# Optimization experiments

Hardware: AMD Instinct MI355X
Metric: run time of the kernel (lower is better)

Reference implementation:

```python
import jax, jax.numpy as jnp
import numpy as np

U = 512   # units
D = 512   # decoder input feature dim
V = 46    # output vocab


def _lstm_cell(x_t, h, c, W, R, b):
    # Keras LSTMCell: gate order i, f, g(cell), o; sigmoid recurrent act, tanh act.
    z = x_t @ W + h @ R + b                      # [B, 4U]
    i, f, g, o = jnp.split(z, 4, axis=-1)
    i = jax.nn.sigmoid(i)
    f = jax.nn.sigmoid(f)
    g = jnp.tanh(g)
    o = jax.nn.sigmoid(o)
    c_new = f * c + i * g
    h_new = o * jnp.tanh(c_new)
    return h_new, c_new


def _lstm_seq(seq, W, R, b):
    # seq: [T, B, D]; zero initial state (Keras default). Returns (all h [T,B,U], last h [B,U]).
    B = seq.shape[1]
    u = R.shape[0]
    h0 = jnp.zeros((B, u), seq.dtype)
    c0 = jnp.zeros((B, u), seq.dtype)
    def step(carry, x_t):
        h, c = carry
        h, c = _lstm_cell(x_t, h, c, W, R, b)
        return (h, c), h
    (hT, _), hs = jax.lax.scan(step, (h0, c0), seq)
    return hs, hT


def setup_inputs() -> dict:
    key = jax.random.key(0)
    ks = jax.random.split(key, 10)
    def p(k, shape, scale=0.05):
        return jax.random.normal(k, shape, dtype=jnp.float32) * scale
    x = jax.random.normal(ks[0], (32, 512, U), dtype=jnp.float32)   # encoder outputs [B, S, U]
    y = jax.random.normal(ks[1], (32, 128, D), dtype=jnp.float32)   # decoder inputs  [B, T, D]
    return {
        "x": x, "y": y,
        "W_a": p(ks[2], (D, 4 * U)), "R_a": p(ks[3], (U, 4 * U)), "b_a": jnp.zeros((4 * U,), jnp.float32),
        "W1": p(ks[4], (U, 4 * U)), "R1": p(ks[5], (U, 4 * U)), "b1": jnp.zeros((4 * U,), jnp.float32),
        "W2": p(ks[6], (U, 4 * U)), "R2": p(ks[7], (U, 4 * U)), "b2": jnp.zeros((4 * U,), jnp.float32),
        "Wd": p(ks[8], (U, V)), "bd": jnp.zeros((V,), jnp.float32),
    }


def reference(x, y, W_a, R_a, b_a, W1, R1, b1, W2, R2, b2, Wd, bd):
    B = y.shape[0]
    yT = jnp.swapaxes(y, 0, 1)                          # [T, B, D]
    h0 = jnp.zeros((B, U), x.dtype)
    c0 = jnp.zeros((B, U), x.dtype)

    # AttentionLSTM: per-step LSTMCell + dot-product attention (Keras Attention,
    # unscaled, keys==values==x) + residual add of the context into both states.
    def step(carry, y_t):
        h, c = carry
        h, c = _lstm_cell(y_t, h, c, W_a, R_a, b_a)     # s = h  [B, U]
        scores = jnp.einsum('bu,bsu->bs', h, x)         # [B, S]
        ctx = jnp.einsum('bs,bsu->bu', jax.nn.softmax(scores, axis=-1), x)  # [B, U]
        return (h + ctx, c + ctx), ctx

    _, ctxs = jax.lax.scan(step, (h0, c0), yT)          # [T, B, U]

    # Stacked LSTMs: first returns full sequence, second returns last hidden state.
    hs1, _ = _lstm_seq(ctxs, W1, R1, b1)                # [T, B, U]
    _, hT = _lstm_seq(hs1, W2, R2, b2)                  # [B, U]

    logits = hT @ Wd + bd                               # [B, V]
    return jax.nn.softmax(logits, axis=-1)
```

## Files before the change

### kernel.cpp

```cpp
#include <hip/hip_runtime.h>
#include <math.h>


#define U_   512
#define S_   512
#define T_   128
#define B_   32
#define G4   2048
#define V_   46
#define NWG  256
#define FSTR 32

#define AT_LD(p)     __hip_atomic_load((p), __ATOMIC_RELAXED, __HIP_MEMORY_SCOPE_AGENT)
#define AT_ST(p, v)  __hip_atomic_store((p), (v), __ATOMIC_RELAXED, __HIP_MEMORY_SCOPE_AGENT)

__device__ __forceinline__ void group_bar(unsigned* gflags, unsigned seq) {
  __syncthreads();
  const int tid = threadIdx.x;
  if (tid < 32) {
    if (tid == 0)
      AT_ST(&gflags[(blockIdx.x & 31) * FSTR], seq);
    while (!__all(AT_LD(&gflags[tid * FSTR]) >= seq))
      __builtin_amdgcn_s_sleep(1);
  }
  __syncthreads();
}

__global__ __launch_bounds__(256) void gemm_k512(
    const float* __restrict__ A, const float* __restrict__ W,
    const float* __restrict__ b, float* __restrict__ Z) {
  const int tid = threadIdx.x;
  const int j = blockIdx.x * 1024 + tid * 4;
  const int i0 = blockIdx.y * 8;
  float4 bj = *(const float4*)(b + j);
  float4 acc[8];
#pragma unroll
  for (int r = 0; r < 8; ++r) acc[r] = bj;
  const float* Arow = A + (size_t)i0 * U_;
  for (int k = 0; k < U_; ++k) {
    float4 w = *(const float4*)(W + (size_t)k * G4 + j);
#pragma unroll
    for (int r = 0; r < 8; ++r) {
      float a = Arow[(size_t)r * U_ + k];
      acc[r].x = fmaf(a, w.x, acc[r].x);
      acc[r].y = fmaf(a, w.y, acc[r].y);
      acc[r].z = fmaf(a, w.z, acc[r].z);
      acc[r].w = fmaf(a, w.w, acc[r].w);
    }
  }
#pragma unroll
  for (int r = 0; r < 8; ++r)
    *(float4*)(Z + (size_t)(i0 + r) * G4 + j) = acc[r];
}

__global__ __launch_bounds__(256) void transpose_R(
    const float* __restrict__ R, float* __restrict__ RT) {
  __shared__ float tile[64][65];
  const int c0 = blockIdx.x * 64, k0 = blockIdx.y * 64;
  const int tc = threadIdx.x & 63, tr = threadIdx.x >> 6;
  for (int r = tr; r < 64; r += 4)
    tile[r][tc] = R[(size_t)(k0 + r) * G4 + c0 + tc];
  __syncthreads();
  for (int r = tr; r < 64; r += 4)
    RT[(size_t)(c0 + r) * 512 + k0 + tc] = tile[tc][r];
}

__global__ __launch_bounds__(512) void attn_coop(
    const float* __restrict__ x, const float* __restrict__ ZY,
    const float* __restrict__ RT, float* __restrict__ ctxs,
    float* hbuf, float* hnbuf, float* smax, float* ssumg,
    float* ctxpart, unsigned* flags) {
  extern __shared__ float dyn[];
  float* x_s  = dyn;
  float* h_st = dyn + 512 * 65;
  __shared__ float zp[4][64][2];
  __shared__ float p_s[64];
  __shared__ float ctx_s[64];

  const int tid = threadIdx.x;
  const int bid = blockIdx.x;
  const int g    = bid >> 5;
  const int wgid = bid & 31;
  const int u0   = wgid * 16;
  const int kh  = tid & 1;
  const int b_l = (tid >> 1) & 3;
  const int col = tid >> 3;
  const int zcol = (col >> 4) * 512 + u0 + (col & 15);
  const int b_att = 4 * g + (wgid >> 3);
  const int sc = wgid & 7;
  unsigned* gflags = flags + g * 32 * FSTR;

  for (int idx = tid; idx < 64 * 512; idx += 512) {
    int sl = idx >> 9, u = idx & 511;
    x_s[u * 65 + sl] = x[((size_t)b_att * S_ + sc * 64 + sl) * U_ + u];
  }
  float c = 0.f, hn_reg = 0.f;
  unsigned seq = 0;
  __syncthreads();

  for (int t = 0; t < T_; ++t) {
    {
      float4 v = make_float4(0.f, 0.f, 0.f, 0.f);
      if (t) {
        const float4* hb4 =
            (const float4*)(hbuf + (size_t)t * 16384 + 4 * g * 512);
        v = hb4[tid];
      }
      *(float4*)(h_st + (tid >> 7) * 516 + (tid & 127) * 4) = v;
    }
    __syncthreads();
    {
      const float4* H4 = (const float4*)(h_st + b_l * 516 + kh * 256);
      const float4* R4 = (const float4*)(RT + (size_t)zcol * 512 + kh * 256);
      float acc = 0.f;
#pragma unroll 8
      for (int i = 0; i < 64; ++i) {
        float4 hv = H4[i];
        float4 rv = R4[i];
        acc = fmaf(hv.x, rv.x, acc); acc = fmaf(hv.y, rv.y, acc);
        acc = fmaf(hv.z, rv.z, acc); acc = fmaf(hv.w, rv.w, acc);
      }
      zp[b_l][col][kh] = acc;
    }
    __syncthreads();
    if (tid < 64) {
      const int bb = tid >> 4, uu = tid & 15;
      const int b = 4 * g + bb, u = u0 + uu;
      const float* zy = ZY + ((size_t)b * T_ + t) * G4 + u;
      float zi = zy[0]    + zp[bb][uu][0]      + zp[bb][uu][1];
      float zf = zy[512]  + zp[bb][16 + uu][0] + zp[bb][16 + uu][1];
      float zg = zy[1024] + zp[bb][32 + uu][0] + zp[bb][32 + uu][1];
      float zo = zy[1536] + zp[bb][48 + uu][0] + zp[bb][48 + uu][1];
      float ig = 1.f / (1.f + expf(-zi));
      float fg = 1.f / (1.f + expf(-zf));
      float gg = tanhf(zg);
      float og = 1.f / (1.f + expf(-zo));
      c = fg * c + ig * gg;
      hn_reg = og * tanhf(c);
      AT_ST(&hnbuf[(size_t)t * 16384 + b * 512 + u], hn_reg);
    }
    group_bar(gflags, ++seq);

    {
      const int wv = tid >> 6, ln = tid & 63;
      const float* hnb = hnbuf + (size_t)t * 16384 + b_att * 512;
      float hreg[8];
#pragma unroll
      for (int k = 0; k < 8; ++k) hreg[k] = hnb[ln + 64 * k];
      for (int si = 0; si < 8; ++si) {
        const int sl = wv * 8 + si;
        float a = 0.f;
#pragma unroll
        for (int k = 0; k < 8; ++k)
          a = fmaf(hreg[k], x_s[(ln + 64 * k) * 65 + sl], a);
#pragma unroll
        for (int off = 32; off; off >>= 1) a += __shfl_down(a, off);
        if (ln == 0) p_s[sl] = a;
      }
    }
    __syncthreads();
    if (tid < 64) {
      float v = p_s[tid];
      float m = v;
#pragma unroll
      for (int off = 32; off; off >>= 1) m = fmaxf(m, __shfl_down(m, off));
      m = __shfl(m, 0);
      float ex = expf(v - m);
      p_s[tid] = ex;
      float sm = ex;
#pragma unroll
      for (int off = 32; off; off >>= 1) sm += __shfl_down(sm, off);
      if (tid == 0) {
        AT_ST(&smax[b_att * 8 + sc], m);
        AT_ST(&ssumg[b_att * 8 + sc], sm);
      }
    }
    __syncthreads();
    {
      float a = 0.f;
      const float* xr = x_s + tid * 65;
#pragma unroll 8
      for (int s = 0; s < 64; ++s) a = fmaf(p_s[s], xr[s], a);
      AT_ST(&ctxpart[((size_t)b_att * 8 + sc) * 512 + tid], a);
    }
    group_bar(gflags, ++seq);

    {
      const int j = tid & 7;
      const int pair = tid >> 3;
      const int bb = pair >> 4, uu = pair & 15;
      const int b = 4 * g + bb, u = u0 + uu;
      float lm = AT_LD(&smax[b * 8 + j]);
      float ss = AT_LD(&ssumg[b * 8 + j]);
      float cp = AT_LD(&ctxpart[((size_t)b * 8 + j) * 512 + u]);
      float gm = lm;
#pragma unroll
      for (int off = 1; off < 8; off <<= 1)
        gm = fmaxf(gm, __shfl_xor(gm, off));
      float w = expf(lm - gm);
      float st = ss * w, cs = cp * w;
#pragma unroll
      for (int off = 1; off < 8; off <<= 1) {
        st += __shfl_xor(st, off);
        cs += __shfl_xor(cs, off);
      }
      if (j == 0) ctx_s[pair] = cs / st;
    }
    __syncthreads();
    if (tid < 64) {
      const int bb = tid >> 4, uu = tid & 15;
      const int b = 4 * g + bb, u = u0 + uu;
      float ctxv = ctx_s[tid];
      c += ctxv;
      float hcar = hn_reg + ctxv;
      AT_ST(&hbuf[(size_t)(t + 1) * 16384 + b * 512 + u], hcar);
      ctxs[((size_t)b * T_ + t) * U_ + u] = ctxv;
    }
    group_bar(gflags, ++seq);
  }
}

__global__ __launch_bounds__(512) void lstm_coop(
    const float* __restrict__ Zin, const float* __restrict__ R,
    float* __restrict__ seq_out, float* hbuf, unsigned* flags,
    const float* __restrict__ Wd, const float* __restrict__ bd,
    float* __restrict__ out) {
  extern __shared__ float dyn[];
  float* R_s  = dyn;
  float* h_st = dyn + 64 * 516;
  __shared__ float zp[4][64][2];
  const int tid = threadIdx.x;
  const int bid = blockIdx.x;
  const int g    = bid >> 5;
  const int wgid = bid & 31;
  const int u0   = wgid * 16;
  const int kh  = tid & 1;
  const int b_l = (tid >> 1) & 3;
  const int col = tid >> 3;
  unsigned* gflags = flags + g * 32 * FSTR;

  for (int idx = tid; idx < 64 * 512; idx += 512) {
    int cc = idx & 63, kk = idx >> 6;
    R_s[cc * 516 + kk] = R[(size_t)kk * G4 + (cc >> 4) * 512 + u0 + (cc & 15)];
  }
  float c = 0.f;
  unsigned seq = 0;
  __syncthreads();

  for (int t = 0; t < T_; ++t) {
    {
      float4 v = make_float4(0.f, 0.f, 0.f, 0.f);
      if (t) {
        const float4* hb4 =
            (const float4*)(hbuf + (size_t)t * 16384 + 4 * g * 512);
        v = hb4[tid];
      }
      *(float4*)(h_st + (tid >> 7) * 516 + (tid & 127) * 4) = v;
    }
    __syncthreads();
    {
      const float4* H4 = (const float4*)(h_st + b_l * 516 + kh * 256);
      const float4* R4 = (const float4*)(R_s + col * 516 + kh * 256);
      float acc = 0.f;
#pragma unroll 8
      for (int i = 0; i < 64; ++i) {
        float4 hv = H4[i];
        float4 rv = R4[i];
        acc = fmaf(hv.x, rv.x, acc); acc = fmaf(hv.y, rv.y, acc);
        acc = fmaf(hv.z, rv.z, acc); acc = fmaf(hv.w, rv.w, acc);
      }
      zp[b_l][col][kh] = acc;
    }
    __syncthreads();
    if (tid < 64) {
      const int bb = tid >> 4, uu = tid & 15;
      const int b = 4 * g + bb, u = u0 + uu;
      const float* zy = Zin + ((size_t)b * T_ + t) * G4 + u;
      float zi = zy[0]    + zp[bb][uu][0]      + zp[bb][uu][1];
      float zf = zy[512]  + zp[bb][16 + uu][0] + zp[bb][16 + uu][1];
      float zg = zy[1024] + zp[bb][32 + uu][0] + zp[bb][32 + uu][1];
      float zo = zy[1536] + zp[bb][48 + uu][0] + zp[bb][48 + uu][1];
      float ig = 1.f / (1.f + expf(-zi));
      float fg = 1.f / (1.f + expf(-zf));
      float gg = tanhf(zg);
      float og = 1.f / (1.f + expf(-zo));
      c = fg * c + ig * gg;
      float hv2 = og * tanhf(c);
      AT_ST(&hbuf[(size_t)(t + 1) * 16384 + b * 512 + u], hv2);
      if (seq_out) seq_out[((size_t)b * T_ + t) * U_ + u] = hv2;
    }
    group_bar(gflags, ++seq);
  }

  if (Wd && wgid == 0 && tid < 256) {
    const int b = 4 * g + (tid >> 6);
    const int v = tid & 63;
    const float* hT = hbuf + (size_t)T_ * 16384 + (size_t)b * 512;
    float acc = (v < V_) ? bd[v] : -INFINITY;
    if (v < V_) {
      for (int k = 0; k < U_; ++k)
        acc = fmaf(hT[k], Wd[(size_t)k * V_ + v], acc);
    }
    float m = acc;
#pragma unroll
    for (int off = 32; off; off >>= 1) m = fmaxf(m, __shfl_down(m, off));
    m = __shfl(m, 0);
    float e = (v < V_) ? expf(acc - m) : 0.f;
    float s = e;
#pragma unroll
    for (int off = 32; off; off >>= 1) s += __shfl_down(s, off);
    s = __shfl(s, 0);
    if (v < V_) out[(size_t)b * V_ + v] = e / s;
  }
}

extern "C" void kernel_launch(void* const* d_in, const int* in_sizes, int n_in,
                              void* d_out, int out_size, void* d_ws, size_t ws_size,
                              hipStream_t stream) {
  const float* x   = (const float*)d_in[0];
  const float* y   = (const float*)d_in[1];
  const float* W_a = (const float*)d_in[2];
  const float* R_a = (const float*)d_in[3];
  const float* b_a = (const float*)d_in[4];
  const float* W1  = (const float*)d_in[5];
  const float* R1  = (const float*)d_in[6];
  const float* b1  = (const float*)d_in[7];
  const float* W2  = (const float*)d_in[8];
  const float* R2  = (const float*)d_in[9];
  const float* b2  = (const float*)d_in[10];
  const float* Wd  = (const float*)d_in[11];
  const float* bd  = (const float*)d_in[12];
  float* out = (float*)d_out;

  float* ZBUF  = (float*)d_ws;
  float* SEQ   = ZBUF + (size_t)8388608;
  float* RT    = SEQ + (size_t)2097152;
  float* HROT  = RT + (size_t)1048576;
  float* HNROT = HROT + (size_t)2113536;
  float* SMAX  = HNROT + (size_t)2097152;
  float* SSUM  = SMAX + 256;
  float* CTXP  = SSUM + 256;
  float* HT    = CTXP + 131072;
  unsigned* BAR = (unsigned*)(HT + 16384);

  const int REGION = 8 * 32 * FSTR;
  unsigned* FLG_A = BAR;
  unsigned* FLG_1 = BAR + REGION;
  unsigned* FLG_2 = BAR + 2 * REGION;

  const int attn_lds = (512 * 65 + 4 * 516) * 4;
  const int lstm_lds = (64 * 516 + 4 * 516) * 4;
  hipFuncSetAttribute((const void*)attn_coop,
                      hipFuncAttributeMaxDynamicSharedMemorySize, attn_lds);
  hipFuncSetAttribute((const void*)lstm_coop,
                      hipFuncAttributeMaxDynamicSharedMemorySize, lstm_lds);

  dim3 ggrid(2, 512);
  hipMemsetAsync(BAR, 0, 3 * REGION * 4, stream);

  gemm_k512<<<ggrid, 256, 0, stream>>>(y, W_a, b_a, ZBUF);
  transpose_R<<<dim3(32, 8), 256, 0, stream>>>(R_a, RT);
  attn_coop<<<NWG, 512, attn_lds, stream>>>(x, ZBUF, RT, SEQ, HROT, HNROT,
                                            SMAX, SSUM, CTXP, FLG_A);
  gemm_k512<<<ggrid, 256, 0, stream>>>(SEQ, W1, b1, ZBUF);
  lstm_coop<<<NWG, 512, lstm_lds, stream>>>(ZBUF, R1, SEQ, HROT, FLG_1,
                                            nullptr, nullptr, nullptr);
  gemm_k512<<<ggrid, 256, 0, stream>>>(SEQ, W2, b2, ZBUF);
  lstm_coop<<<NWG, 512, lstm_lds, stream>>>(ZBUF, R2, nullptr, HROT, FLG_2,
                                            Wd, bd, out);
}
```

Baseline: 4.037 ms.

## Fuse attention and both stacked LSTMs into one wavefront-pipelined persistent kernel

```diff
diff --git a/kernel.cpp b/kernel.cpp
--- a/kernel.cpp
+++ b/kernel.cpp
@@ -8,23 +8,10 @@
 #define B_   32
 #define G4   2048
 #define V_   46
-#define NWG  256
 #define FSTR 32
 
 #define AT_LD(p)     __hip_atomic_load((p), __ATOMIC_RELAXED, __HIP_MEMORY_SCOPE_AGENT)
 #define AT_ST(p, v)  __hip_atomic_store((p), (v), __ATOMIC_RELAXED, __HIP_MEMORY_SCOPE_AGENT)
-
-__device__ __forceinline__ void group_bar(unsigned* gflags, unsigned seq) {
-  __syncthreads();
-  const int tid = threadIdx.x;
-  if (tid < 32) {
-    if (tid == 0)
-      AT_ST(&gflags[(blockIdx.x & 31) * FSTR], seq);
-    while (!__all(AT_LD(&gflags[tid * FSTR]) >= seq))
-      __builtin_amdgcn_s_sleep(1);
-  }
-  __syncthreads();
-}
 
 __global__ __launch_bounds__(256) void gemm_k512(
     const float* __restrict__ A, const float* __restrict__ W,
@@ -65,65 +52,81 @@
     RT[(size_t)(c0 + r) * 512 + k0 + tc] = tile[tc][r];
 }
 
-__global__ __launch_bounds__(512) void attn_coop(
+__global__ __launch_bounds__(1024) void mega(
     const float* __restrict__ x, const float* __restrict__ ZY,
-    const float* __restrict__ RT, float* __restrict__ ctxs,
-    float* hbuf, float* hnbuf, float* smax, float* ssumg,
-    float* ctxpart, unsigned* flags) {
+    const float* __restrict__ RT,
+    const float* __restrict__ W1T, const float* __restrict__ R1T,
+    const float* __restrict__ b1,
+    const float* __restrict__ W2T, const float* __restrict__ R2T,
+    const float* __restrict__ b2,
+    const float* __restrict__ Wd, const float* __restrict__ bd,
+    float* ctxs, float* hbuf, float* hnbuf, float* h1rot, float* h2rot,
+    float* smax, float* ssumg, float* ctxpart,
+    float* __restrict__ out, unsigned* flagsA, unsigned* flags1) {
   extern __shared__ float dyn[];
   float* x_s  = dyn;
   float* h_st = dyn + 512 * 65;
   __shared__ float zp[4][64][2];
   __shared__ float p_s[64];
   __shared__ float ctx_s[64];
+  __shared__ float zp1[4][64];
+  __shared__ float zp2[4][64];
 
   const int tid = threadIdx.x;
   const int bid = blockIdx.x;
   const int g    = bid >> 5;
   const int wgid = bid & 31;
   const int u0   = wgid * 16;
+  unsigned* gfA = flagsA + g * 32 * FSTR;
+  unsigned* gf1 = flags1 + g * 32 * FSTR;
+
   const int kh  = tid & 1;
   const int b_l = (tid >> 1) & 3;
   const int col = tid >> 3;
-  const int zcol = (col >> 4) * 512 + u0 + (col & 15);
+  const int zcolA = (col >> 4) * 512 + u0 + (col & 15);
   const int b_att = 4 * g + (wgid >> 3);
   const int sc = wgid & 7;
-  unsigned* gflags = flags + g * 32 * FSTR;
-
-  for (int idx = tid; idx < 64 * 512; idx += 512) {
+
+  const int ct  = tid & 255;
+  const int cbl = ct & 3;
+  const int ccl = ct >> 2;
+  const int czc = (ccl >> 4) * 512 + u0 + (ccl & 15);
+  const int cb  = 4 * g + cbl;
+
+  for (int idx = tid; idx < 64 * 512; idx += 1024) {
     int sl = idx >> 9, u = idx & 511;
     x_s[u * 65 + sl] = x[((size_t)b_att * S_ + sc * 64 + sl) * U_ + u];
   }
   float c = 0.f, hn_reg = 0.f;
-  unsigned seq = 0;
+  float c1 = 0.f, c2 = 0.f;
   __syncthreads();
 
-  for (int t = 0; t < T_; ++t) {
-    {
+  for (int t = 0; t < T_ + 4; ++t) {
+    const bool aON = (t < T_);
+    const int s1 = t - 2; const bool l1 = (s1 >= 0) && (s1 < T_);
+    const int s2 = t - 4; const bool l2 = (s2 >= 0) && (s2 < T_);
+    float w1a = 0.f, w2a = 0.f;
+
+    if (aON && tid < 512) {
       float4 v = make_float4(0.f, 0.f, 0.f, 0.f);
-      if (t) {
-        const float4* hb4 =
-            (const float4*)(hbuf + (size_t)t * 16384 + 4 * g * 512);
-        v = hb4[tid];
-      }
+      if (t) v = ((const float4*)(hbuf + (size_t)t * 16384 + 4 * g * 512))[tid];
       *(float4*)(h_st + (tid >> 7) * 516 + (tid & 127) * 4) = v;
     }
     __syncthreads();
-    {
+    if (aON && tid < 512) {
       const float4* H4 = (const float4*)(h_st + b_l * 516 + kh * 256);
-      const float4* R4 = (const float4*)(RT + (size_t)zcol * 512 + kh * 256);
+      const float4* R4 = (const float4*)(RT + (size_t)zcolA * 512 + kh * 256);
       float acc = 0.f;
 #pragma unroll 8
       for (int i = 0; i < 64; ++i) {
-        float4 hv = H4[i];
-        float4 rv = R4[i];
+        float4 hv = H4[i]; float4 rv = R4[i];
         acc = fmaf(hv.x, rv.x, acc); acc = fmaf(hv.y, rv.y, acc);
         acc = fmaf(hv.z, rv.z, acc); acc = fmaf(hv.w, rv.w, acc);
       }
       zp[b_l][col][kh] = acc;
     }
     __syncthreads();
-    if (tid < 64) {
+    if (aON && tid < 64) {
       const int bb = tid >> 4, uu = tid & 15;
       const int b = 4 * g + bb, u = u0 + uu;
       const float* zy = ZY + ((size_t)b * T_ + t) * G4 + u;
@@ -139,9 +142,39 @@
       hn_reg = og * tanhf(c);
       AT_ST(&hnbuf[(size_t)t * 16384 + b * 512 + u], hn_reg);
     }
-    group_bar(gflags, ++seq);
-
-    {
+    __syncthreads();
+    if (aON && tid < 32) {
+      if (tid == 0) AT_ST(&gfA[wgid * FSTR], 3u * t + 1u);
+      while (!__all(AT_LD(&gfA[tid * FSTR]) >= 3u * t + 1u))
+        __builtin_amdgcn_s_sleep(1);
+    }
+    if (l1 && tid >= 512 && tid < 768) {
+      const float4* W4 = (const float4*)(W1T + (size_t)czc * 512);
+      const float4* X4 = (const float4*)(ctxs + ((size_t)cb * T_ + s1) * U_);
+      float a = 0.f;
+#pragma unroll 8
+      for (int i = 0; i < 128; ++i) {
+        float4 wv = W4[i]; float4 xv = X4[i];
+        a = fmaf(xv.x, wv.x, a); a = fmaf(xv.y, wv.y, a);
+        a = fmaf(xv.z, wv.z, a); a = fmaf(xv.w, wv.w, a);
+      }
+      w1a = a;
+    }
+    if (l2 && tid >= 768) {
+      const float4* W4 = (const float4*)(W2T + (size_t)czc * 512);
+      const float4* H4 =
+          (const float4*)(h1rot + (size_t)(s2 + 1) * 16384 + (size_t)cb * 512);
+      float a = 0.f;
+#pragma unroll 8
+      for (int i = 0; i < 128; ++i) {
+        float4 wv = W4[i]; float4 hv = H4[i];
+        a = fmaf(hv.x, wv.x, a); a = fmaf(hv.y, wv.y, a);
+        a = fmaf(hv.z, wv.z, a); a = fmaf(hv.w, wv.w, a);
+      }
+      w2a = a;
+    }
+    __syncthreads();
+    if (aON && tid < 512) {
       const int wv = tid >> 6, ln = tid & 63;
       const float* hnb = hnbuf + (size_t)t * 16384 + b_att * 512;
       float hreg[8];
@@ -159,7 +192,7 @@
       }
     }
     __syncthreads();
-    if (tid < 64) {
+    if (aON && tid < 64) {
       float v = p_s[tid];
       float m = v;
 #pragma unroll
@@ -176,16 +209,51 @@
       }
     }
     __syncthreads();
-    {
+    if (aON && tid < 512) {
       float a = 0.f;
       const float* xr = x_s + tid * 65;
 #pragma unroll 8
       for (int s = 0; s < 64; ++s) a = fmaf(p_s[s], xr[s], a);
       AT_ST(&ctxpart[((size_t)b_att * 8 + sc) * 512 + tid], a);
     }
-    group_bar(gflags, ++seq);
-
-    {
+    __syncthreads();
+    if (aON && tid < 32) {
+      if (tid == 0) AT_ST(&gfA[wgid * FSTR], 3u * t + 2u);
+      while (!__all(AT_LD(&gfA[tid * FSTR]) >= 3u * t + 2u))
+        __builtin_amdgcn_s_sleep(1);
+    }
+    if (l1 && tid >= 512 && tid < 768) {
+      float a = 0.f;
+      if (s1) {
+        const float4* R4 = (const float4*)(R1T + (size_t)czc * 512);
+        const float4* H4 =
+            (const float4*)(h1rot + (size_t)s1 * 16384 + (size_t)cb * 512);
+#pragma unroll 8
+        for (int i = 0; i < 128; ++i) {
+          float4 rv = R4[i]; float4 hv = H4[i];
+          a = fmaf(hv.x, rv.x, a); a = fmaf(hv.y, rv.y, a);
+          a = fmaf(hv.z, rv.z, a); a = fmaf(hv.w, rv.w, a);
+        }
+      }
+      zp1[cbl][ccl] = w1a + a;
+    }
+    if (l2 && tid >= 768) {
+      float a = 0.f;
+      if (s2) {
+        const float4* R4 = (const float4*)(R2T + (size_t)czc * 512);
+        const float4* H4 =
+            (const float4*)(h2rot + (size_t)s2 * 16384 + (size_t)cb * 512);
+#pragma unroll 8
+        for (int i = 0; i < 128; ++i) {
+          float4 rv = R4[i]; float4 hv = H4[i];
+          a = fmaf(hv.x, rv.x, a); a = fmaf(hv.y, rv.y, a);
+          a = fmaf(hv.z, rv.z, a); a = fmaf(hv.w, rv.w, a);
+        }
+      }
+      zp2[cbl][ccl] = w2a + a;
+    }
+    __syncthreads();
+    if (aON && tid < 512) {
       const int j = tid & 7;
       const int pair = tid >> 3;
       const int bb = pair >> 4, uu = pair & 15;
@@ -207,95 +275,70 @@
       if (j == 0) ctx_s[pair] = cs / st;
     }
     __syncthreads();
-    if (tid < 64) {
+    if (aON && tid < 64) {
       const int bb = tid >> 4, uu = tid & 15;
       const int b = 4 * g + bb, u = u0 + uu;
       float ctxv = ctx_s[tid];
       c += ctxv;
       float hcar = hn_reg + ctxv;
       AT_ST(&hbuf[(size_t)(t + 1) * 16384 + b * 512 + u], hcar);
-      ctxs[((size_t)b * T_ + t) * U_ + u] = ctxv;
-    }
-    group_bar(gflags, ++seq);
-  }
-}
-
-__global__ __launch_bounds__(512) void lstm_coop(
-    const float* __restrict__ Zin, const float* __restrict__ R,
-    float* __restrict__ seq_out, float* hbuf, unsigned* flags,
-    const float* __restrict__ Wd, const float* __restrict__ bd,
-    float* __restrict__ out) {
-  extern __shared__ float dyn[];
-  float* R_s  = dyn;
-  float* h_st = dyn + 64 * 516;
-  __shared__ float zp[4][64][2];
-  const int tid = threadIdx.x;
-  const int bid = blockIdx.x;
-  const int g    = bid >> 5;
-  const int wgid = bid & 31;
-  const int u0   = wgid * 16;
-  const int kh  = tid & 1;
-  const int b_l = (tid >> 1) & 3;
-  const int col = tid >> 3;
-  unsigned* gflags = flags + g * 32 * FSTR;
-
-  for (int idx = tid; idx < 64 * 512; idx += 512) {
-    int cc = idx & 63, kk = idx >> 6;
-    R_s[cc * 516 + kk] = R[(size_t)kk * G4 + (cc >> 4) * 512 + u0 + (cc & 15)];
-  }
-  float c = 0.f;
-  unsigned seq = 0;
-  __syncthreads();
-
-  for (int t = 0; t < T_; ++t) {
-    {
-      float4 v = make_float4(0.f, 0.f, 0.f, 0.f);
-      if (t) {
-        const float4* hb4 =
-            (const float4*)(hbuf + (size_t)t * 16384 + 4 * g * 512);
-        v = hb4[tid];
-      }
-      *(float4*)(h_st + (tid >> 7) * 516 + (tid & 127) * 4) = v;
-    }
-    __syncthreads();
-    {
-      const float4* H4 = (const float4*)(h_st + b_l * 516 + kh * 256);
-      const float4* R4 = (const float4*)(R_s + col * 516 + kh * 256);
-      float acc = 0.f;
-#pragma unroll 8
-      for (int i = 0; i < 64; ++i) {
-        float4 hv = H4[i];
-        float4 rv = R4[i];
-        acc = fmaf(hv.x, rv.x, acc); acc = fmaf(hv.y, rv.y, acc);
-        acc = fmaf(hv.z, rv.z, acc); acc = fmaf(hv.w, rv.w, acc);
-      }
-      zp[b_l][col][kh] = acc;
-    }
-    __syncthreads();
-    if (tid < 64) {
-      const int bb = tid >> 4, uu = tid & 15;
+      AT_ST(&ctxs[((size_t)b * T_ + t) * U_ + u], ctxv);
+    }
+    if (l1 && tid >= 512 && tid < 576) {
+      const int cc = tid - 512;
+      const int bb = cc >> 4, uu = cc & 15;
       const int b = 4 * g + bb, u = u0 + uu;
-      const float* zy = Zin + ((size_t)b * T_ + t) * G4 + u;
-      float zi = zy[0]    + zp[bb][uu][0]      + zp[bb][uu][1];
-      float zf = zy[512]  + zp[bb][16 + uu][0] + zp[bb][16 + uu][1];
-      float zg = zy[1024] + zp[bb][32 + uu][0] + zp[bb][32 + uu][1];
-      float zo = zy[1536] + zp[bb][48 + uu][0] + zp[bb][48 + uu][1];
+      float zi = b1[u]        + zp1[bb][uu];
+      float zf = b1[512 + u]  + zp1[bb][16 + uu];
+      float zg = b1[1024 + u] + zp1[bb][32 + uu];
+      float zo = b1[1536 + u] + zp1[bb][48 + uu];
       float ig = 1.f / (1.f + expf(-zi));
       float fg = 1.f / (1.f + expf(-zf));
       float gg = tanhf(zg);
       float og = 1.f / (1.f + expf(-zo));
-      c = fg * c + ig * gg;
-      float hv2 = og * tanhf(c);
-      AT_ST(&hbuf[(size_t)(t + 1) * 16384 + b * 512 + u], hv2);
-      if (seq_out) seq_out[((size_t)b * T_ + t) * U_ + u] = hv2;
-    }
-    group_bar(gflags, ++seq);
+      c1 = fg * c1 + ig * gg;
+      float hv = og * tanhf(c1);
+      AT_ST(&h1rot[(size_t)(s1 + 1) * 16384 + (size_t)b * 512 + u], hv);
+    }
+    if (l2 && tid >= 768 && tid < 832) {
+      const int cc = tid - 768;
+      const int bb = cc >> 4, uu = cc & 15;
+      const int b = 4 * g + bb, u = u0 + uu;
+      float zi = b2[u]        + zp2[bb][uu];
+      float zf = b2[512 + u]  + zp2[bb][16 + uu];
+      float zg = b2[1024 + u] + zp2[bb][32 + uu];
+      float zo = b2[1536 + u] + zp2[bb][48 + uu];
+      float ig = 1.f / (1.f + expf(-zi));
+      float fg = 1.f / (1.f + expf(-zf));
+      float gg = tanhf(zg);
+      float og = 1.f / (1.f + expf(-zo));
+      c2 = fg * c2 + ig * gg;
+      float hv = og * tanhf(c2);
+      AT_ST(&h2rot[(size_t)(s2 + 1) * 16384 + (size_t)b * 512 + u], hv);
+    }
+    __syncthreads();
+    if (aON && tid < 32) {
+      if (tid == 0) AT_ST(&gfA[wgid * FSTR], 3u * t + 3u);
+      while (!__all(AT_LD(&gfA[tid * FSTR]) >= 3u * t + 3u))
+        __builtin_amdgcn_s_sleep(1);
+    }
+    __syncthreads();
+    if (t >= T_) {
+      if (tid < 32) {
+        unsigned dseq = (unsigned)(t - T_ + 1);
+        if (tid == 0) AT_ST(&gf1[wgid * FSTR], dseq);
+        while (!__all(AT_LD(&gf1[tid * FSTR]) >= dseq))
+          __builtin_amdgcn_s_sleep(1);
+      }
+      __syncthreads();
+    }
   }
 
-  if (Wd && wgid == 0 && tid < 256) {
-    const int b = 4 * g + (tid >> 6);
-    const int v = tid & 63;
-    const float* hT = hbuf + (size_t)T_ * 16384 + (size_t)b * 512;
+  if (wgid == 0 && tid >= 512 && tid < 768) {
+    const int cc = tid - 512;
+    const int b = 4 * g + (cc >> 6);
+    const int v = cc & 63;
+    const float* hT = h2rot + (size_t)T_ * 16384 + (size_t)b * 512;
     float acc = (v < V_) ? bd[v] : -INFINITY;
     if (v < V_) {
       for (int k = 0; k < U_; ++k)
@@ -333,39 +376,40 @@
   float* out = (float*)d_out;
 
   float* ZBUF  = (float*)d_ws;
-  float* SEQ   = ZBUF + (size_t)8388608;
-  float* RT    = SEQ + (size_t)2097152;
-  float* HROT  = RT + (size_t)1048576;
+  float* CTXS  = ZBUF + (size_t)8388608;
+  float* RT    = CTXS + (size_t)2097152;
+  float* W1T   = RT + (size_t)1048576;
+  float* R1T   = W1T + (size_t)1048576;
+  float* W2T   = R1T + (size_t)1048576;
+  float* R2T   = W2T + (size_t)1048576;
+  float* HROT  = R2T + (size_t)1048576;
   float* HNROT = HROT + (size_t)2113536;
-  float* SMAX  = HNROT + (size_t)2097152;
+  float* H1ROT = HNROT + (size_t)2097152;
+  float* H2ROT = H1ROT + (size_t)2113536;
+  float* SMAX  = H2ROT + (size_t)2113536;
   float* SSUM  = SMAX + 256;
   float* CTXP  = SSUM + 256;
-  float* HT    = CTXP + 131072;
-  unsigned* BAR = (unsigned*)(HT + 16384);
+  unsigned* BAR = (unsigned*)(CTXP + 131072);
 
   const int REGION = 8 * 32 * FSTR;
   unsigned* FLG_A = BAR;
   unsigned* FLG_1 = BAR + REGION;
-  unsigned* FLG_2 = BAR + 2 * REGION;
-
-  const int attn_lds = (512 * 65 + 4 * 516) * 4;
-  const int lstm_lds = (64 * 516 + 4 * 516) * 4;
-  hipFuncSetAttribute((const void*)attn_coop,
-                      hipFuncAttributeMaxDynamicSharedMemorySize, attn_lds);
-  hipFuncSetAttribute((const void*)lstm_coop,
-                      hipFuncAttributeMaxDynamicSharedMemorySize, lstm_lds);
+
+  const int mega_lds = (512 * 65 + 4 * 516) * 4;
+  hipFuncSetAttribute((const void*)mega,
+                      hipFuncAttributeMaxDynamicSharedMemorySize, mega_lds);
 
   dim3 ggrid(2, 512);
-  hipMemsetAsync(BAR, 0, 3 * REGION * 4, stream);
+  hipMemsetAsync(BAR, 0, 2 * REGION * 4, stream);
 
   gemm_k512<<<ggrid, 256, 0, stream>>>(y, W_a, b_a, ZBUF);
   transpose_R<<<dim3(32, 8), 256, 0, stream>>>(R_a, RT);
-  attn_coop<<<NWG, 512, attn_lds, stream>>>(x, ZBUF, RT, SEQ, HROT, HNROT,
-                                            SMAX, SSUM, CTXP, FLG_A);
-  gemm_k512<<<ggrid, 256, 0, stream>>>(SEQ, W1, b1, ZBUF);
-  lstm_coop<<<NWG, 512, lstm_lds, stream>>>(ZBUF, R1, SEQ, HROT, FLG_1,
-                                            nullptr, nullptr, nullptr);
-  gemm_k512<<<ggrid, 256, 0, stream>>>(SEQ, W2, b2, ZBUF);
-  lstm_coop<<<NWG, 512, lstm_lds, stream>>>(ZBUF, R2, nullptr, HROT, FLG_2,
-                                            Wd, bd, out);
+  transpose_R<<<dim3(32, 8), 256, 0, stream>>>(W1, W1T);
+  transpose_R<<<dim3(32, 8), 256, 0, stream>>>(R1, R1T);
+  transpose_R<<<dim3(32, 8), 256, 0, stream>>>(W2, W2T);
+  transpose_R<<<dim3(32, 8), 256, 0, stream>>>(R2, R2T);
+  mega<<<256, 1024, mega_lds, stream>>>(x, ZBUF, RT, W1T, R1T, b1,
+                                        W2T, R2T, b2, Wd, bd,
+                                        CTXS, HROT, HNROT, H1ROT, H2ROT,
+                                        SMAX, SSUM, CTXP, out, FLG_A, FLG_1);
 }
```

Result: slower. 11.14 ms (+175.9%).
